# Optimization experiments

Measured on AMD Instinct MI355X. Metric: run time of the kernel, lower is better.

The kernel has to match this reference:

```python
import jax, jax.numpy as jnp
import numpy as np

N_WIRES = 10
N_OPS = 30
C64 = jnp.complex64

# Frozen random circuit (stand-in for tq.RandomLayer(n_ops=30)): deterministic op list.
_rng = np.random.default_rng(42)
OPS = []
for _ in range(N_OPS):
    k = int(_rng.integers(0, 4))
    if k == 3:
        w = _rng.choice(N_WIRES, size=2, replace=False)
        OPS.append(('cnot', int(w[0]), int(w[1])))
    else:
        OPS.append((('rx', 'ry', 'rz')[k], int(_rng.integers(0, N_WIRES)), -1))


def _rx_mat(t):
    c = jnp.cos(t / 2).astype(C64)
    s = jnp.sin(t / 2).astype(C64)
    return jnp.stack([jnp.stack([c, -1j * s]), jnp.stack([-1j * s, c])])


def _ry_mat(t):
    c = jnp.cos(t / 2).astype(C64)
    s = jnp.sin(t / 2).astype(C64)
    return jnp.stack([jnp.stack([c, -s]), jnp.stack([s, c])])


def _rz_mat(t):
    tc = t.astype(C64)
    z = jnp.zeros((), C64)
    return jnp.stack([jnp.stack([jnp.exp(-1j * tc / 2), z]), jnp.stack([z, jnp.exp(1j * tc / 2)])])

_GATE = {'rx': _rx_mat, 'ry': _ry_mat, 'rz': _rz_mat}


def _apply_1q(state, U, w):
    # state: [bsz] + [2]*N_WIRES ; apply 2x2 U on qubit axis w
    s = jnp.moveaxis(state, 1 + w, -1)
    s = jnp.einsum('ij,...j->...i', U, s)
    return jnp.moveaxis(s, -1, 1 + w)


def _apply_cnot(state, c, t):
    s = jnp.moveaxis(state, (1 + c, 1 + t), (-2, -1))
    s = jnp.stack([s[..., 0, :], s[..., 1, ::-1]], axis=-2)  # flip target when control=1
    return jnp.moveaxis(s, (-2, -1), (1 + c, 1 + t))


def _quantum_head(x, rand_params, rx_theta, ry_theta, head_w, head_b):
    bsz = x.shape[0]
    # GeneralEncoder '10xRy': RY(x[:,w])|0> per wire -> product state built directly
    state = jnp.ones((bsz, 1), C64)
    for w in range(N_WIRES):
        vec = jnp.stack([jnp.cos(x[:, w] / 2), jnp.sin(x[:, w] / 2)], axis=-1).astype(C64)
        state = (state[:, :, None] * vec[:, None, :]).reshape(bsz, -1)
    state = state.reshape((bsz,) + (2,) * N_WIRES)
    # RandomLayer (frozen 30-op circuit, one angle per op)
    for i, (kind, a, b) in enumerate(OPS):
        if kind == 'cnot':
            state = _apply_cnot(state, a, b)
        else:
            state = _apply_1q(state, _GATE[kind](rand_params[i]), a)
    # shared trainable RX then RY applied to every wire (single shared param each)
    Urx = _rx_mat(rx_theta[0])
    Ury = _ry_mat(ry_theta[0])
    for w in range(N_WIRES):
        state = _apply_1q(state, Urx, w)
        state = _apply_1q(state, Ury, w)
    # MeasureAll(PauliZ): <Z_w> = P(bit_w=0) - P(bit_w=1)
    probs = jnp.abs(state) ** 2  # float32, [bsz] + [2]*n
    feats = []
    for w in range(N_WIRES):
        axes = tuple(1 + q for q in range(N_WIRES) if q != w)
        p = probs.sum(axis=axes)  # [bsz, 2]
        feats.append(p[:, 0] - p[:, 1])
    feats = jnp.stack(feats, axis=-1)  # [bsz, n_wires]
    return feats @ head_w + head_b[0]


def _mlp(x, w0, b0, w1, b1, w2, b2, w3, b3):
    # faithful to ClassicalMLP: Linear chain with NO activations
    h = x @ w0.T + b0
    h = h @ w1.T + b1
    h = h @ w2.T + b2
    return (h @ w3.T + b3)[:, 0]


def setup_inputs() -> dict:
    key = jax.random.key(0)
    ks = jax.random.split(key, 14)
    BSZ = 8192
    return {
        'state_batch': jax.random.normal(ks[0], (BSZ, N_WIRES), jnp.float32),
        'rand_params': jax.random.normal(ks[1], (N_OPS,), jnp.float32),
        'rx_theta': jax.random.normal(ks[2], (1,), jnp.float32),
        'ry_theta': jax.random.normal(ks[3], (1,), jnp.float32),
        'head_w': jax.random.normal(ks[4], (N_WIRES,), jnp.float32) * 0.3,
        'head_b': jax.random.normal(ks[5], (1,), jnp.float32) * 0.1,
        'w0': jax.random.normal(ks[6], (64, N_WIRES), jnp.float32) * 0.3,
        'b0': jax.random.normal(ks[7], (64,), jnp.float32) * 0.1,
        'w1': jax.random.normal(ks[8], (32, 64), jnp.float32) * 0.12,
        'b1': jax.random.normal(ks[9], (32,), jnp.float32) * 0.1,
        'w2': jax.random.normal(ks[10], (16, 32), jnp.float32) * 0.17,
        'b2': jax.random.normal(ks[11], (16,), jnp.float32) * 0.1,
        'w3': jax.random.normal(ks[12], (1, 16), jnp.float32) * 0.25,
        'b3': jax.random.normal(ks[13], (1,), jnp.float32) * 0.1,
    }


def reference(state_batch, rand_params, rx_theta, ry_theta, head_w, head_b, w0, b0, w1, b1, w2, b2, w3, b3):
    q = _quantum_head(state_batch, rand_params, rx_theta, ry_theta, head_w, head_b)
    c = _mlp(state_batch, w0, b0, w1, b1, w2, b2, w3, b3)
    return q + c
```

## Files before the change

kernel.cpp:

```cpp
#include <hip/hip_runtime.h>
#include <cstdint>

#define NW 10
#define NOPS 30

namespace {

typedef unsigned __int128 u128;

struct CRng { u128 state; u128 inc; bool has32; uint32_t cached; };

constexpr u128 PCG_MUL = (((u128)0x2360ED051FC65DA4ULL) << 64) | (u128)0x4385DF649FCCF645ULL;

constexpr void cr_step(CRng &r) { r.state = r.state * PCG_MUL + r.inc; }

constexpr uint64_t cr_out(u128 st) {
  uint64_t hi = (uint64_t)(st >> 64);
  uint64_t lo = (uint64_t)st;
  unsigned rot = (unsigned)(st >> 122) & 63u;
  uint64_t v = hi ^ lo;
  return (v >> rot) | (v << ((64u - rot) & 63u));
}

constexpr uint64_t cr_next64(CRng &r) { cr_step(r); return cr_out(r.state); }

constexpr uint32_t cr_next32(CRng &r) {
  if (r.has32) { r.has32 = false; return r.cached; }
  uint64_t v = cr_next64(r);
  r.has32 = true; r.cached = (uint32_t)(v >> 32);
  return (uint32_t)v;
}

constexpr CRng cr_seed(uint32_t ent) {
  uint32_t pool[4] = {0u, 0u, 0u, 0u};
  uint32_t hc = 0x43b0d7e5u;
  for (int i = 0; i < 4; i++) {
    uint32_t v = (i == 0) ? ent : 0u;
    v ^= hc; hc *= 0x931e8875u; v *= hc; v ^= v >> 16;
    pool[i] = v;
  }
  for (int s = 0; s < 4; s++)
    for (int d = 0; d < 4; d++)
      if (s != d) {
        uint32_t v = pool[s];
        v ^= hc; hc *= 0x931e8875u; v *= hc; v ^= v >> 16;
        uint32_t res = 0xca01f9ddu * pool[d] - 0x4973f715u * v;
        res ^= res >> 16;
        pool[d] = res;
      }
  uint32_t hb = 0x8b51f9ddu;
  uint64_t s64[4] = {0ull, 0ull, 0ull, 0ull};
  for (int i = 0; i < 8; i++) {
    uint32_t d = pool[i & 3];
    d ^= hb; hb *= 0x58f38dedu; d *= hb; d ^= d >> 16;
    if (i & 1) s64[i >> 1] |= ((uint64_t)d << 32); else s64[i >> 1] = (uint64_t)d;
  }
  CRng r{};
  u128 initstate = (((u128)s64[0]) << 64) | (u128)s64[1];
  u128 initseq   = (((u128)s64[2]) << 64) | (u128)s64[3];
  r.state = 0; r.inc = (initseq << 1) | (u128)1;
  cr_step(r);
  r.state += initstate;
  cr_step(r);
  r.has32 = false; r.cached = 0u;
  return r;
}

constexpr uint32_t cr_lemire32(CRng &r, uint32_t rng) {
  uint32_t rng_excl = rng + 1u;
  uint64_t m = (uint64_t)cr_next32(r) * (uint64_t)rng_excl;
  uint32_t leftover = (uint32_t)m;
  if (leftover < rng_excl) {
    uint32_t threshold = (uint32_t)(0xFFFFFFFFu - rng) % rng_excl;
    while (leftover < threshold) {
      m = (uint64_t)cr_next32(r) * (uint64_t)rng_excl;
      leftover = (uint32_t)m;
    }
  }
  return (uint32_t)(m >> 32);
}

constexpr bool canary_pcg42() {
  CRng r = cr_seed(42u);
  double a = (double)(cr_next64(r) >> 11) * (1.0 / 9007199254740992.0);
  double b = (double)(cr_next64(r) >> 11) * (1.0 / 9007199254740992.0);
  double c = (double)(cr_next64(r) >> 11) * (1.0 / 9007199254740992.0);
  bool ok = (a > 0.77395603) && (a < 0.77395607);
  ok = ok && (b > 0.43887842) && (b < 0.43887846);
  ok = ok && (c > 0.85859790) && (c < 0.85859794);
  return ok;
}
static_assert(canary_pcg42(), "CANARY_PCG_SEED42_RANDOM_MISMATCH");

struct COp { int kind; int a; int b; int slot; };
struct Circ { COp op[NOPS]; };

constexpr Circ build_circuit() {
  Circ c{};
  CRng r = cr_seed(42u);
  for (int i = 0; i < NOPS; i++) {
    int k = (int)cr_lemire32(r, 3u);
    if (k == 3) {
      uint32_t v8 = cr_lemire32(r, 8u);
      uint32_t v9 = cr_lemire32(r, 9u);
      uint32_t i0 = v8;
      uint32_t i1 = (v9 == v8) ? 9u : v9;
      uint32_t j = cr_lemire32(r, 1u);
      if (j == 0u) { uint32_t t = i0; i0 = i1; i1 = t; }
      c.op[i] = COp{3, (int)i0, (int)i1, i};
    } else {
      int w = (int)cr_lemire32(r, 9u);
      c.op[i] = COp{k, w, 0, i};
    }
  }
  return c;
}
constexpr Circ CC = build_circuit();

constexpr int MAXP = 16384;
constexpr int MAXU = 4096;

struct Tables {
  int np, nu, overflow;
  uint32_t pmeta[MAXP]; uint32_t pcm[MAXP]; uint32_t psm[MAXP];
  uint32_t ukey[MAXU];  int ustart[MAXU + 1];
  uint32_t upk[MAXU];
};

constexpr Tables build_tables() {
  Tables T{};
  uint32_t meta[MAXP] = {}; uint32_t cm[MAXP] = {}; uint32_t sm[MAXP] = {};
  int np = 0; int ovf = 0;
  for (int w = 0; w < NW; w++)
    for (int src = 0; src < 3; src++) {
      uint32_t xm = (src != 0) ? (1u << w) : 0u;
      uint32_t zm = (src != 1) ? (1u << w) : 0u;
      meta[np] = xm | (zm << 10) | ((uint32_t)w << 21) | ((uint32_t)src << 25);
      cm[np] = 0u; sm[np] = 0u; np++;
    }
  for (int k = NOPS - 1; k >= 0 && !ovf; k--) {
    const COp op = CC.op[k];
    if (op.kind == 3) {
      const int c = op.a, t = op.b;
      for (int p = 0; p < np; p++) {
        uint32_t m = meta[p];
        uint32_t xm = m & 1023u, zm = (m >> 10) & 1023u;
        uint32_t xc = (xm >> c) & 1u, zc = (zm >> c) & 1u;
        uint32_t xt = (xm >> t) & 1u, zt = (zm >> t) & 1u;
        uint32_t fl = xc & zt & (1u ^ (xt ^ zc));
        xm ^= xc << t;
        zm ^= zt << c;
        m = (m & ~(1023u | (1023u << 10))) | xm | (zm << 10);
        m ^= fl << 20;
        meta[p] = m;
      }
    } else {
      const int q = op.a, ax = op.kind, bit = op.slot;
      const int n0 = np;
      for (int p = 0; p < n0; p++) {
        uint32_t m = meta[p];
        uint32_t x = (m >> q) & 1u;
        uint32_t z = (m >> (10 + q)) & 1u;
        uint32_t viol = (ax == 0) ? z : (ax == 1) ? (x ^ z) : x;
        if (viol) {
          uint32_t nx = 0, nz = 0, fl = 0;
          if (ax == 0)      { if (x) { nx = 0; nz = 1; fl = 1; } else { nx = 1; nz = 1; fl = 0; } }
          else if (ax == 1) { if (x) { nx = 0; nz = 1; fl = 0; } else { nx = 1; nz = 0; fl = 1; } }
          else              { if (z) { nx = 1; nz = 0; fl = 0; } else { nx = 1; nz = 1; fl = 1; } }
          if (np >= MAXP) { ovf = 1; break; }
          uint32_t m2 = m;
          m2 &= ~((1u << q) | (1u << (10 + q)));
          m2 |= (nx << q) | (nz << (10 + q));
          m2 ^= fl << 20;
          meta[np] = m2; cm[np] = cm[p]; sm[np] = sm[p] | (1u << bit);
          np++;
          cm[p] |= 1u << bit;
        }
      }
    }
  }
  if (ovf) { T.overflow = 1; return T; }
  int n2 = 0;
  for (int p = 0; p < np; p++) {
    uint32_t m = meta[p];
    if ((m & 1023u) & ((m >> 10) & 1023u)) continue;
    meta[n2] = m; cm[n2] = cm[p]; sm[n2] = sm[p]; n2++;
  }
  np = n2;
  int idx[MAXP] = {}; int tmp[MAXP] = {};
  for (int i = 0; i < np; i++) idx[i] = i;
  int hist[1025] = {};
  for (int i = 0; i < 1025; i++) hist[i] = 0;
  for (int i = 0; i < np; i++) hist[1 + (meta[idx[i]] & 1023u)]++;
  for (int i = 0; i < 1024; i++) hist[i + 1] += hist[i];
  for (int i = 0; i < np; i++) tmp[hist[meta[idx[i]] & 1023u]++] = idx[i];
  for (int i = 0; i < 1025; i++) hist[i] = 0;
  for (int i = 0; i < np; i++) hist[1 + ((meta[tmp[i]] >> 10) & 1023u)]++;
  for (int i = 0; i < 1024; i++) hist[i + 1] += hist[i];
  for (int i = 0; i < np; i++) idx[hist[(meta[tmp[i]] >> 10) & 1023u]++] = tmp[i];
  int nu = 0; uint32_t prev = 0xFFFFFFFFu;
  for (int i = 0; i < np; i++) {
    int p = idx[i];
    uint32_t key = meta[p] & 0xFFFFFu;
    if (key != prev) {
      if (nu >= MAXU) { T.overflow = 2; return T; }
      T.ukey[nu] = key; T.ustart[nu] = i; prev = key; nu++;
    }
    T.pmeta[i] = meta[p]; T.pcm[i] = cm[p]; T.psm[i] = sm[p];
  }
  T.ustart[nu] = np;
  for (int u = 0; u < nu; u++) {
    uint32_t key = T.ukey[u]; uint32_t pk = 0;
    for (int p = 0; p < 5; p++) {
      uint32_t x2 = (key >> (2 * p)) & 3u;
      uint32_t z2 = (key >> (10 + 2 * p)) & 3u;
      pk |= ((x2 | (z2 << 2)) << 2) << (6 * p);
    }
    T.upk[u] = pk;
  }
  T.np = np; T.nu = nu; T.overflow = 0;
  return T;
}

constexpr Tables TT = build_tables();
static_assert(TT.overflow == 0, "PAULI_PATH_OVERFLOW_raise_MAXP_or_pivot_to_runtime_tables");
static_assert(TT.nu >= 1 && TT.nu <= MAXU, "PAULI_UNIQUE_COUNT_OUT_OF_RANGE");
constexpr int NU  = TT.nu;
constexpr int NUP = (NU + 1) & ~1;

}

__device__ const Tables dTT = TT;

__global__ __launch_bounds__(256) void prep_kernel(
    const float* __restrict__ rand_params,
    const float* __restrict__ rx_theta, const float* __restrict__ ry_theta,
    const float* __restrict__ head_w, const float* __restrict__ head_b,
    const float* __restrict__ w0, const float* __restrict__ b0,
    const float* __restrict__ w1, const float* __restrict__ b1,
    const float* __restrict__ w2, const float* __restrict__ b2,
    const float* __restrict__ w3, const float* __restrict__ b3,
    float* __restrict__ ws)
{
  const int tid = threadIdx.x;
  __shared__ float ct[32], st[32], abr[3], hwsh[10];
  __shared__ float r2[32], r1[64];

  if (tid < NOPS) {
    float t = rand_params[tid];
    ct[tid] = cosf(t);
    st[tid] = sinf(t);
  }
  if (tid == 30) {
    float tx = rx_theta[0], ty = ry_theta[0];
    abr[0] = cosf(tx) * cosf(ty);
    abr[1] = -sinf(ty);
    abr[2] = sinf(tx) * cosf(ty);
  }
  if (tid < NW) hwsh[tid] = head_w[tid];
  __syncthreads();

  const int u = blockIdx.x * 256 + tid;
  float2* ws2 = (float2*)ws;
  if (u < NU) {
    float acc = 0.f;
    const int i0 = dTT.ustart[u], i1 = dTT.ustart[u + 1];
    for (int i = i0; i < i1; i++) {
      uint32_t m = dTT.pmeta[i];
      float v = hwsh[(m >> 21) & 15u] * abr[(m >> 25) & 3u];
      if (m & (1u << 20)) v = -v;
      uint32_t c = dTT.pcm[i];
      while (c) { int b = __builtin_ctz(c); v *= ct[b]; c &= c - 1u; }
      uint32_t s = dTT.psm[i];
      while (s) { int b = __builtin_ctz(s); v *= st[b]; s &= s - 1u; }
      acc += v;
    }
    ws2[u] = make_float2(acc, __uint_as_float(dTT.upk[u]));
  } else if (u < NUP) {
    ws2[u] = make_float2(0.f, __uint_as_float(0u));
  }

  if (blockIdx.x == 0) {
    if (tid < 32) {
      float acc = 0.f;
      for (int k = 0; k < 16; k++) acc += w3[k] * w2[k * 32 + tid];
      r2[tid] = acc;
    }
    __syncthreads();
    if (tid < 64) {
      float acc = 0.f;
      for (int k = 0; k < 32; k++) acc += r2[k] * w1[k * 64 + tid];
      r1[tid] = acc;
    }
    __syncthreads();
    if (tid < NW) {
      float acc = 0.f;
      for (int k = 0; k < 64; k++) acc += r1[k] * w0[k * NW + tid];
      ws[2 * NUP + tid] = acc;
    }
    if (tid == NW) {
      float acc = b3[0] + head_b[0];
      for (int k = 0; k < 16; k++) acc += w3[k] * b2[k];
      for (int k = 0; k < 32; k++) acc += r2[k] * b1[k];
      for (int k = 0; k < 64; k++) acc += r1[k] * b0[k];
      ws[2 * NUP + NW] = acc;
    }
  }
}

__global__ __launch_bounds__(256) void qsim_kernel(
    const float* __restrict__ x,
    const float* __restrict__ ws,
    float* __restrict__ out,
    int bsz)
{
  __shared__ __align__(16) float2 CKsh[NUP];
  __shared__ float Tbl[4][80];
  __shared__ float MLPsh[NW + 1];
  const int tid = threadIdx.x;
  const float2* ws2 = (const float2*)ws;
  for (int i = tid; i < NUP; i += 256) CKsh[i] = ws2[i];
  if (tid < NW + 1) MLPsh[tid] = ws[2 * NUP + tid];

  const int wv = (int)((blockIdx.x * blockDim.x + tid) >> 6);
  const int lane = tid & 63;
  float* tbl = Tbl[tid >> 6];
  const bool live = (wv < bsz);
  const float* xe = x + wv * NW;

  if (live) {
    {
      const int e = lane;
      const int p = e >> 4, code = e & 15;
      float2 xv = *(const float2*)(xe + 2 * p);
      float c0 = __cosf(xv.x), s0 = __sinf(xv.x);
      float c1 = __cosf(xv.y), s1 = __sinf(xv.y);
      float f0 = (code & 1) ? s0 : ((code & 4) ? c0 : 1.0f);
      float f1 = (code & 2) ? s1 : ((code & 8) ? c1 : 1.0f);
      tbl[e] = f0 * f1;
    }
    if (lane < 16) {
      const int e = lane + 64;
      const int p = e >> 4, code = e & 15;
      float2 xv = *(const float2*)(xe + 2 * p);
      float c0 = __cosf(xv.x), s0 = __sinf(xv.x);
      float c1 = __cosf(xv.y), s1 = __sinf(xv.y);
      float f0 = (code & 1) ? s0 : ((code & 4) ? c0 : 1.0f);
      float f1 = (code & 2) ? s1 : ((code & 8) ? c1 : 1.0f);
      tbl[e] = f0 * f1;
    }
  }
  __syncthreads();
  if (!live) return;

  const char* tb = (const char*)tbl;
  float acc0 = 0.f, acc1 = 0.f;
#pragma unroll 4
  for (int s = 2 * lane; s < NUP; s += 128) {
    float4 q = *(const float4*)&CKsh[s];
    uint32_t ka = __float_as_uint(q.y);
    uint32_t kb = __float_as_uint(q.w);
    float a0 = *(const float*)(tb +       ( ka        & 63u));
    float a1 = *(const float*)(tb +  64 + ((ka >>  6) & 63u));
    float a2 = *(const float*)(tb + 128 + ((ka >> 12) & 63u));
    float a3 = *(const float*)(tb + 192 + ((ka >> 18) & 63u));
    float a4 = *(const float*)(tb + 256 + ((ka >> 24) & 63u));
    float b0 = *(const float*)(tb +       ( kb        & 63u));
    float b1 = *(const float*)(tb +  64 + ((kb >>  6) & 63u));
    float b2 = *(const float*)(tb + 128 + ((kb >> 12) & 63u));
    float b3 = *(const float*)(tb + 192 + ((kb >> 18) & 63u));
    float b4 = *(const float*)(tb + 256 + ((kb >> 24) & 63u));
    acc0 = fmaf(q.x, ((a0 * a1) * (a2 * a3)) * a4, acc0);
    acc1 = fmaf(q.z, ((b0 * b1) * (b2 * b3)) * b4, acc1);
  }
  float acc = acc0 + acc1;

#pragma unroll
  for (int m = 1; m < 64; m <<= 1) acc += __shfl_xor(acc, m);

  if (lane == 0) {
    float cc = MLPsh[NW];
#pragma unroll
    for (int w = 0; w < NW; w++) cc += xe[w] * MLPsh[w];
    out[wv] = acc + cc;
  }
}

extern "C" void kernel_launch(void* const* d_in, const int* in_sizes, int n_in,
                              void* d_out, int out_size, void* d_ws, size_t ws_size,
                              hipStream_t stream) {
  const float* x   = (const float*)d_in[0];
  const float* rp  = (const float*)d_in[1];
  const float* rxT = (const float*)d_in[2];
  const float* ryT = (const float*)d_in[3];
  const float* hw  = (const float*)d_in[4];
  const float* hb  = (const float*)d_in[5];
  const float* w0  = (const float*)d_in[6];
  const float* b0  = (const float*)d_in[7];
  const float* w1  = (const float*)d_in[8];
  const float* b1  = (const float*)d_in[9];
  const float* w2  = (const float*)d_in[10];
  const float* b2  = (const float*)d_in[11];
  const float* w3  = (const float*)d_in[12];
  const float* b3  = (const float*)d_in[13];
  const int bsz = in_sizes[0] / NW;

  float* ws = (float*)d_ws;

  const int prep_blocks = (NUP + 255) / 256;
  hipLaunchKernelGGL(prep_kernel, dim3(prep_blocks), dim3(256), 0, stream,
                     rp, rxT, ryT, hw, hb, w0, b0, w1, b1, w2, b2, w3, b3, ws);

  const int blocks = (bsz + 3) / 4;
  hipLaunchKernelGGL(qsim_kernel, dim3(blocks), dim3(256), 0, stream,
                     x, ws, (float*)d_out, bsz);
}
```

Baseline: 94.80 us.

## Fuse coefficient prep and simulation into one kernel with 1024-thread blocks

Merges the prep kernel, which built Pauli-path coefficients and the folded MLP weights, into the simulation kernel. Each block now recomputes the coefficient table and MLP reduction into shared memory itself, so the second launch and the workspace round trip disappear. Blocks grow to 1024 threads with 16 waves each to spread that per-block recomputation over more batch elements. The cost is that every block repeats the prep work and holds a larger block, which can reduce occupancy.

Result: slower. 100.4 us (+5.9%).

```diff
diff --git a/kernel.cpp b/kernel.cpp
--- a/kernel.cpp
+++ b/kernel.cpp
@@ -232,7 +232,11 @@
 
 __device__ const Tables dTT = TT;
 
-__global__ __launch_bounds__(256) void prep_kernel(
+#define BLOCK 1024
+#define WPB   16
+
+__global__ __launch_bounds__(BLOCK) void fused_kernel(
+    const float* __restrict__ x,
     const float* __restrict__ rand_params,
     const float* __restrict__ rx_theta, const float* __restrict__ ry_theta,
     const float* __restrict__ head_w, const float* __restrict__ head_b,
@@ -240,29 +244,38 @@
     const float* __restrict__ w1, const float* __restrict__ b1,
     const float* __restrict__ w2, const float* __restrict__ b2,
     const float* __restrict__ w3, const float* __restrict__ b3,
-    float* __restrict__ ws)
+    float* __restrict__ out, int bsz)
 {
-  const int tid = threadIdx.x;
+  __shared__ __align__(16) float2 CKsh[NUP];
+  __shared__ float Tbl[WPB][80];
   __shared__ float ct[32], st[32], abr[3], hwsh[10];
   __shared__ float r2[32], r1[64];
+  __shared__ float MLPsh[NW + 1];
+
+  const int tid  = threadIdx.x;
+  const int wave = tid >> 6;
+  const int lane = tid & 63;
 
   if (tid < NOPS) {
     float t = rand_params[tid];
     ct[tid] = cosf(t);
     st[tid] = sinf(t);
-  }
-  if (tid == 30) {
+  } else if (tid == 32) {
     float tx = rx_theta[0], ty = ry_theta[0];
     abr[0] = cosf(tx) * cosf(ty);
     abr[1] = -sinf(ty);
     abr[2] = sinf(tx) * cosf(ty);
-  }
-  if (tid < NW) hwsh[tid] = head_w[tid];
+  } else if (tid >= 64 && tid < 96) {
+    const int j = tid - 64;
+    float acc = 0.f;
+    for (int k = 0; k < 16; k++) acc += w3[k] * w2[k * 32 + j];
+    r2[j] = acc;
+  } else if (tid >= 96 && tid < 96 + NW) {
+    hwsh[tid - 96] = head_w[tid - 96];
+  }
   __syncthreads();
 
-  const int u = blockIdx.x * 256 + tid;
-  float2* ws2 = (float2*)ws;
-  if (u < NU) {
+  for (int u = tid; u < NU; u += BLOCK) {
     float acc = 0.f;
     const int i0 = dTT.ustart[u], i1 = dTT.ustart[u + 1];
     for (int i = i0; i < i1; i++) {
@@ -275,59 +288,33 @@
       while (s) { int b = __builtin_ctz(s); v *= st[b]; s &= s - 1u; }
       acc += v;
     }
-    ws2[u] = make_float2(acc, __uint_as_float(dTT.upk[u]));
-  } else if (u < NUP) {
-    ws2[u] = make_float2(0.f, __uint_as_float(0u));
-  }
-
-  if (blockIdx.x == 0) {
-    if (tid < 32) {
-      float acc = 0.f;
-      for (int k = 0; k < 16; k++) acc += w3[k] * w2[k * 32 + tid];
-      r2[tid] = acc;
-    }
-    __syncthreads();
-    if (tid < 64) {
-      float acc = 0.f;
-      for (int k = 0; k < 32; k++) acc += r2[k] * w1[k * 64 + tid];
-      r1[tid] = acc;
-    }
-    __syncthreads();
-    if (tid < NW) {
-      float acc = 0.f;
-      for (int k = 0; k < 64; k++) acc += r1[k] * w0[k * NW + tid];
-      ws[2 * NUP + tid] = acc;
-    }
-    if (tid == NW) {
-      float acc = b3[0] + head_b[0];
-      for (int k = 0; k < 16; k++) acc += w3[k] * b2[k];
-      for (int k = 0; k < 32; k++) acc += r2[k] * b1[k];
-      for (int k = 0; k < 64; k++) acc += r1[k] * b0[k];
-      ws[2 * NUP + NW] = acc;
-    }
-  }
-}
-
-__global__ __launch_bounds__(256) void qsim_kernel(
-    const float* __restrict__ x,
-    const float* __restrict__ ws,
-    float* __restrict__ out,
-    int bsz)
-{
-  __shared__ __align__(16) float2 CKsh[NUP];
-  __shared__ float Tbl[4][80];
-  __shared__ float MLPsh[NW + 1];
-  const int tid = threadIdx.x;
-  const float2* ws2 = (const float2*)ws;
-  for (int i = tid; i < NUP; i += 256) CKsh[i] = ws2[i];
-  if (tid < NW + 1) MLPsh[tid] = ws[2 * NUP + tid];
-
-  const int wv = (int)((blockIdx.x * blockDim.x + tid) >> 6);
-  const int lane = tid & 63;
-  float* tbl = Tbl[tid >> 6];
+    CKsh[u] = make_float2(acc, __uint_as_float(dTT.upk[u]));
+  }
+  if (NU < NUP && tid == 0) CKsh[NU] = make_float2(0.f, __uint_as_float(0u));
+  if (tid >= BLOCK - 64) {
+    const int j = tid - (BLOCK - 64);
+    float acc = 0.f;
+    for (int k = 0; k < 32; k++) acc += r2[k] * w1[k * 64 + j];
+    r1[j] = acc;
+  }
+  __syncthreads();
+
+  if (tid < NW) {
+    float acc = 0.f;
+    for (int k = 0; k < 64; k++) acc += r1[k] * w0[k * NW + tid];
+    MLPsh[tid] = acc;
+  } else if (tid == NW) {
+    float acc = b3[0] + head_b[0];
+    for (int k = 0; k < 16; k++) acc += w3[k] * b2[k];
+    for (int k = 0; k < 32; k++) acc += r2[k] * b1[k];
+    for (int k = 0; k < 64; k++) acc += r1[k] * b0[k];
+    MLPsh[NW] = acc;
+  }
+
+  const int wv = blockIdx.x * WPB + wave;
   const bool live = (wv < bsz);
   const float* xe = x + wv * NW;
-
+  float* tbl = Tbl[wave];
   if (live) {
     {
       const int e = lane;
@@ -365,13 +352,13 @@
     float a2 = *(const float*)(tb + 128 + ((ka >> 12) & 63u));
     float a3 = *(const float*)(tb + 192 + ((ka >> 18) & 63u));
     float a4 = *(const float*)(tb + 256 + ((ka >> 24) & 63u));
-    float b0 = *(const float*)(tb +       ( kb        & 63u));
-    float b1 = *(const float*)(tb +  64 + ((kb >>  6) & 63u));
-    float b2 = *(const float*)(tb + 128 + ((kb >> 12) & 63u));
-    float b3 = *(const float*)(tb + 192 + ((kb >> 18) & 63u));
-    float b4 = *(const float*)(tb + 256 + ((kb >> 24) & 63u));
+    float b0v = *(const float*)(tb +       ( kb        & 63u));
+    float b1v = *(const float*)(tb +  64 + ((kb >>  6) & 63u));
+    float b2v = *(const float*)(tb + 128 + ((kb >> 12) & 63u));
+    float b3v = *(const float*)(tb + 192 + ((kb >> 18) & 63u));
+    float b4v = *(const float*)(tb + 256 + ((kb >> 24) & 63u));
     acc0 = fmaf(q.x, ((a0 * a1) * (a2 * a3)) * a4, acc0);
-    acc1 = fmaf(q.z, ((b0 * b1) * (b2 * b3)) * b4, acc1);
+    acc1 = fmaf(q.z, ((b0v * b1v) * (b2v * b3v)) * b4v, acc1);
   }
   float acc = acc0 + acc1;
 
@@ -405,13 +392,8 @@
   const float* b3  = (const float*)d_in[13];
   const int bsz = in_sizes[0] / NW;
 
-  float* ws = (float*)d_ws;
-
-  const int prep_blocks = (NUP + 255) / 256;
-  hipLaunchKernelGGL(prep_kernel, dim3(prep_blocks), dim3(256), 0, stream,
-                     rp, rxT, ryT, hw, hb, w0, b0, w1, b1, w2, b2, w3, b3, ws);
-
-  const int blocks = (bsz + 3) / 4;
-  hipLaunchKernelGGL(qsim_kernel, dim3(blocks), dim3(256), 0, stream,
-                     x, ws, (float*)d_out, bsz);
-}
+  const int blocks = (bsz + WPB - 1) / WPB;
+  hipLaunchKernelGGL(fused_kernel, dim3(blocks), dim3(BLOCK), 0, stream,
+                     x, rp, rxT, ryT, hw, hb, w0, b0, w1, b1, w2, b2, w3, b3,
+                     (float*)d_out, bsz);
+}
```
